# Performance work log

Measured on AMD Instinct MI355X. Metric: run time of the kernel, lower is better.

## Reference

```python
import jax, jax.numpy as jnp
import numpy as np

GROUPSIZE = 4      # g: multivariate group size (d = groupsize - 2)
NB_GROUPS = 48     # f: number of expert groups / filters
CHANNELS = 128     # c: signal channels fed to the L operator
SCALE = 0.999
SLOPE = 1.0        # model_params['scaling']
LAMB_INIT = 0.1
EPS_OMEGA_INIT = -2.0


def proj_l1(x):
    """Euclidean projection onto the unit l1 ball along axis 1. x: [B,G,F,H,W]."""
    ax = jnp.abs(x)
    s = -jnp.sort(-ax, axis=1)                      # descending |x|
    cssv = jnp.cumsum(s, axis=1) - 1.0
    G = x.shape[1]
    k = jnp.arange(1, G + 1, dtype=x.dtype).reshape(1, G, 1, 1, 1)
    cond = s * k > cssv
    rho = jnp.sum(cond, axis=1, keepdims=True)       # number of active coords
    theta = jnp.take_along_axis(cssv, rho - 1, axis=1) / rho.astype(x.dtype)
    theta = jnp.maximum(theta, 0.0)
    proj = jnp.sign(x) * jnp.maximum(ax - theta, 0.0)
    inside = jnp.sum(ax, axis=1, keepdims=True) <= 1.0
    return jnp.where(inside, x, proj)


def _forward(x_noisy, sigma, Q_param, taus_param, lamb, eps_omega,
             mu_w1, mu_b1, mu_w2, mu_b2, mu_w3, mu_b3, Wf, n_iter):
    lamb_e = jnp.exp(lamb)
    eps_e = jnp.exp(eps_omega)

    # --- Q normalization + spectral norms (cached once per forward) ---
    Q = Q_param / jnp.maximum(jnp.sum(jnp.abs(Q_param), axis=2, keepdims=True), 1.0)
    Q_norms = jnp.linalg.svd(Q, compute_uv=False)[:, 0].reshape(-1, 1, 1)  # [F,1,1]
    Q_eff = Q / Q_norms ** 2
    taus = jnp.exp(jax.nn.relu(taus_param))          # [1,1,F,1,1]

    # --- per-batch noise-adaptive scaling via small MLP ---
    h = jax.nn.relu((sigma * 20.0 - 2.0) @ mu_w1 + mu_b1)
    h = jax.nn.relu(h @ mu_w2 + mu_b2)
    h = h @ mu_w3 + mu_b3                            # [B,F]
    scaling = jax.nn.relu(h * 0.05 + sigma) * SLOPE + 1e-9
    scaling = scaling.reshape(-1, 1, scaling.shape[-1], 1, 1)  # [B,1,F,1,1]

    def moreau(x):
        g = proj_l1(x)
        cost = jnp.max(jnp.abs(x - g), axis=1) + 0.5 * jnp.sum(g * g, axis=1)
        cost = cost[:, None]                         # [B,1,F,H,W]
        g = g + eps_e * x
        cost = cost + eps_e * 0.5 * jnp.sqrt(jnp.sum(x * x, axis=1, keepdims=True))
        return g, cost

    def activation(x):
        gc, cc = moreau(x)
        # orient: scale * einsum('flg,bgfhw->blfhw', Q/Q_norms^2, x), then /taus
        y = SCALE * jnp.einsum('flg,bgfhw->blfhw', Q_eff, x) / taus
        gcc, ccc = moreau(y)
        # unorient: scale * einsum with Q^T  (Q^T[f,l,g] = Q[f,g,l])
        gcc = SCALE * jnp.einsum('fgl,bgfhw->blfhw', Q, gcc)
        ccc = Q_norms ** 2 * (taus * ccc)
        return lamb_e * (gc - gcc), lamb_e * (cc - ccc)

    def reconstruct(x):
        Lx = jnp.einsum('gfc,bchw->bgfhw', Wf, x) / scaling
        g, cost = activation(Lx)
        g = jnp.einsum('gfc,bgfhw->bchw', Wf, g * scaling)   # adjoint L^T
        cost = jnp.sum(cost * scaling ** 2, axis=(1, 2, 3, 4))
        g = (x - x_noisy + g) / (1.0 + lamb_e * (1.0 + eps_e))
        cost = cost + 0.5 * jnp.sum((x - x_noisy) ** 2, axis=(1, 2, 3))
        return g, cost

    def step(x, _):
        g, _c = reconstruct(x)
        return x - g, None

    x_final, _ = jax.lax.scan(jax.checkpoint(step), x_noisy, jnp.arange(n_iter))
    return x_final


def setup_inputs() -> dict:
    key = jax.random.key(0)
    ks = jax.random.split(key, 8)
    B, C, H, W = 2, CHANNELS, 128, 128
    F_, G = NB_GROUPS, GROUPSIZE
    x_noisy = jax.random.normal(ks[0], (B, C, H, W), jnp.float32)
    sigma = jax.random.uniform(ks[1], (B, 1), jnp.float32)
    Q_param = jax.random.uniform(ks[2], (F_, G, G), jnp.float32) - 0.5
    taus_param = (LAMB_INIT / 2.0) * jnp.ones((1, 1, F_, 1, 1), jnp.float32)
    lamb = jnp.float32(LAMB_INIT)
    eps_omega = jnp.float32(EPS_OMEGA_INIT)
    mu_w1 = jax.random.normal(ks[3], (1, F_), jnp.float32)
    mu_b1 = jnp.zeros((F_,), jnp.float32)
    mu_w2 = jax.random.normal(ks[4], (F_, F_), jnp.float32) / np.float32(np.sqrt(F_))
    mu_b2 = jnp.zeros((F_,), jnp.float32)
    mu_w3 = jax.random.normal(ks[5], (F_, F_), jnp.float32) / np.float32(np.sqrt(F_))
    mu_b3 = jnp.zeros((F_,), jnp.float32)
    Wf = jax.random.normal(ks[6], (G, F_, C), jnp.float32) / np.float32(np.sqrt(C))
    return dict(x_noisy=x_noisy, sigma=sigma, Q_param=Q_param, taus_param=taus_param,
                lamb=lamb, eps_omega=eps_omega, mu_w1=mu_w1, mu_b1=mu_b1,
                mu_w2=mu_w2, mu_b2=mu_b2, mu_w3=mu_w3, mu_b3=mu_b3, Wf=Wf, n_iter=10)


def reference(x_noisy, sigma, Q_param, taus_param, lamb, eps_omega,
              mu_w1, mu_b1, mu_w2, mu_b2, mu_w3, mu_b3, Wf, n_iter):
    return _forward(x_noisy, sigma, Q_param, taus_param, lamb, eps_omega,
                    mu_w1, mu_b1, mu_w2, mu_b2, mu_w3, mu_b3, Wf, n_iter)
```

## Files before the change

### kernel.cpp

```cpp
#include <hip/hip_runtime.h>
#include <math.h>

#define F_ 48
#define C_ 128
#define HW 16384
#define SCALE_C 0.999f
#define TPB 256
#define MTPB 512

typedef __attribute__((ext_vector_type(8))) short short8;
typedef __attribute__((ext_vector_type(4))) float floatx4;
typedef __attribute__((ext_vector_type(8))) _Float16 half8;
typedef __attribute__((ext_vector_type(4))) _Float16 half4;

#define P1_U 0
#define P2_U 98304
#define QEQN_F 98304
#define MISC_F (QEQN_F + 1536)
#define SINV_F (MISC_F + 2)
#define SLAM_F (SINV_F + 96)

#define QS 36

__device__ __forceinline__ unsigned short f2bf(float f) {
    unsigned u = __float_as_uint(f);
    unsigned r = u + 0x7fffu + ((u >> 16) & 1u);
    return (unsigned short)(r >> 16);
}
__device__ __forceinline__ float bf2f(unsigned short h) {
    return __uint_as_float(((unsigned)h) << 16);
}

__global__ void setup_math(const float* __restrict__ sigma,
                           const float* __restrict__ Qp,
                           const float* __restrict__ taus_p,
                           const float* __restrict__ lamb,
                           const float* __restrict__ eps_om,
                           const float* __restrict__ mw1, const float* __restrict__ mb1,
                           const float* __restrict__ mw2, const float* __restrict__ mb2,
                           const float* __restrict__ mw3, const float* __restrict__ mb3,
                           float* __restrict__ wsf)
{
    const int tid = threadIdx.x;
    if (tid < F_) {
        const int f = tid;
        float Qm[4][4];
        for (int g = 0; g < 4; ++g) {
            float s = 0.f;
            for (int l = 0; l < 4; ++l) s += fabsf(Qp[f * 16 + g * 4 + l]);
            float d = fmaxf(s, 1.0f);
            for (int l = 0; l < 4; ++l) Qm[g][l] = Qp[f * 16 + g * 4 + l] / d;
        }
        double A[4][4];
        for (int i = 0; i < 4; ++i)
            for (int j = 0; j < 4; ++j) {
                double s = 0.0;
                for (int g = 0; g < 4; ++g) s += (double)Qm[g][i] * (double)Qm[g][j];
                A[i][j] = s;
            }
        double M[4][4];
        for (int i = 0; i < 4; ++i) for (int j = 0; j < 4; ++j) M[i][j] = A[i][j];
        for (int it = 0; it < 30; ++it) {
            double T[4][4]; double mx = 0.0;
            for (int i = 0; i < 4; ++i)
                for (int j = 0; j < 4; ++j) {
                    double s = 0.0;
                    for (int k = 0; k < 4; ++k) s += M[i][k] * M[k][j];
                    T[i][j] = s;
                    double a = fabs(s); if (a > mx) mx = a;
                }
            if (mx < 1e-300) break;
            double inv = 1.0 / mx;
            for (int i = 0; i < 4; ++i) for (int j = 0; j < 4; ++j) M[i][j] = T[i][j] * inv;
        }
        int jb = 0; double bn = -1.0;
        for (int j = 0; j < 4; ++j) {
            double nn = 0.0;
            for (int i = 0; i < 4; ++i) nn += M[i][j] * M[i][j];
            if (nn > bn) { bn = nn; jb = j; }
        }
        double v[4]; for (int i = 0; i < 4; ++i) v[i] = M[i][jb];
        double Av[4];
        for (int i = 0; i < 4; ++i) {
            double s = 0.0;
            for (int j = 0; j < 4; ++j) s += A[i][j] * v[j];
            Av[i] = s;
        }
        double vv = 0.0, vav = 0.0;
        for (int i = 0; i < 4; ++i) { vv += v[i] * v[i]; vav += v[i] * Av[i]; }
        float lamf = (float)((vv > 0.0) ? (vav / vv) : 0.0);
        float tau = expf(fmaxf(taus_p[f], 0.0f));
        float qsv = SCALE_C / tau;
        for (int l = 0; l < 4; ++l)
            for (int g = 0; g < 4; ++g)
                wsf[QEQN_F + f * 32 + l * 4 + g] = qsv * Qm[l][g] / lamf;
        for (int g = 0; g < 4; ++g)
            for (int l = 0; l < 4; ++l)
                wsf[QEQN_F + f * 32 + 16 + g * 4 + l] = SCALE_C * Qm[g][l];
    }
    if (tid >= 48 && tid < 50) {
        const int b = tid - 48;
        float lamb_e = expf(lamb[0]);
        float sg = sigma[b];
        float t = sg * 20.0f - 2.0f;
        float h1[F_], h2[F_];
        for (int j = 0; j < F_; ++j) h1[j] = fmaxf(t * mw1[j] + mb1[j], 0.0f);
        for (int j = 0; j < F_; ++j) {
            float s = mb2[j];
            for (int k = 0; k < F_; ++k) s += h1[k] * mw2[k * F_ + j];
            h2[j] = fmaxf(s, 0.0f);
        }
        for (int j = 0; j < F_; ++j) {
            float s = mb3[j];
            for (int k = 0; k < F_; ++k) s += h2[k] * mw3[k * F_ + j];
            float sc = fmaxf(s * 0.05f + sg, 0.0f) + 1e-9f;
            wsf[SINV_F + b * F_ + j] = 1.0f / sc;
            wsf[SLAM_F + b * F_ + j] = lamb_e * sc;
        }
    }
    if (tid == 50) {
        float lamb_e = expf(lamb[0]);
        float eps_e = expf(eps_om[0]);
        wsf[MISC_F + 0] = eps_e;
        wsf[MISC_F + 1] = 1.0f / (1.0f + lamb_e * (1.0f + eps_e));
    }
}

__global__ void setup_pack(const float* __restrict__ Wf, float* __restrict__ wsf)
{
    unsigned short* wsu = (unsigned short*)wsf;
    const int gtid = blockIdx.x * TPB + threadIdx.x;
    for (int i = gtid; i < 49152; i += gridDim.x * TPB) {
        if (i < 24576) {
            int j = i & 7, lane = (i >> 3) & 63;
            int t = i >> 9;
            int ks = t & 3, mt = t >> 2;
            int m = lane & 15, q = lane >> 4;
            int r = mt * 16 + m;
            int c = ks * 32 + q * 8 + j;
            int f = r >> 2, g = r & 3;
            float w = Wf[(g * F_ + f) * C_ + c];
            _Float16 hv = (_Float16)w;
            wsu[P1_U + ((mt * 4 + ks) * 64 + lane) * 8 + j] = *(unsigned short*)&hv;
        } else {
            int ii = i - 24576;
            int j = ii & 7, lane = (ii >> 3) & 63;
            int t = ii >> 9;
            int ks = t % 6, cmt = t / 6;
            int m = lane & 15, q = lane >> 4;
            int cch = cmt * 16 + m;
            int r = ks * 32 + q * 8 + j;
            int g = r & 3;
            int f = r >> 2;
            float w = Wf[(g * F_ + f) * C_ + cch];
            _Float16 hv = (_Float16)w;
            wsu[P2_U + ((cmt * 6 + ks) * 64 + lane) * 8 + j] = *(unsigned short*)&hv;
        }
    }
}

__device__ __forceinline__ void proj4(const float v[4], float o[4]) {
    float a0 = fabsf(v[0]), a1 = fabsf(v[1]), a2 = fabsf(v[2]), a3 = fabsf(v[3]);
    float sum = a0 + a1 + a2 + a3;
    float t0 = fmaxf(a0, a1), u0 = fminf(a0, a1);
    float t1 = fmaxf(a2, a3), u1 = fminf(a2, a3);
    float s0 = fmaxf(t0, t1), m0 = fminf(t0, t1);
    float m1 = fmaxf(u0, u1), s3 = fminf(u0, u1);
    float s1 = fmaxf(m1, m0), s2 = fminf(m1, m0);
    float c2 = s0 + s1, c3 = c2 + s2, c4 = c3 + s3;
    float th = s0 - 1.0f, rh = 1.0f;
    if (s1 * 2.0f > c2 - 1.0f) { th = c2 - 1.0f; rh = 2.0f; }
    if (s2 * 3.0f > c3 - 1.0f) { th = c3 - 1.0f; rh = 3.0f; }
    if (s3 * 4.0f > c4 - 1.0f) { th = c4 - 1.0f; rh = 4.0f; }
    float theta = fmaxf(th / rh, 0.0f);
    bool inside = (sum <= 1.0f);
#pragma unroll
    for (int g = 0; g < 4; ++g) {
        float ag = fabsf(v[g]);
        float pg = copysignf(fmaxf(ag - theta, 0.0f), v[g]);
        o[g] = inside ? v[g] : pg;
    }
}

__global__ __launch_bounds__(MTPB, 4) void mfoe_main(
    const float* __restrict__ xnoisy,
    const float* __restrict__ wsf,
    float* __restrict__ out,
    const int* __restrict__ n_iter_p)
{
    __shared__ __align__(16) _Float16 sXF[4096];
    __shared__ __align__(16) _Float16 sACT[6144];
    __shared__ __align__(16) float sQ[F_ * QS];

    const int tid = threadIdx.x;
    const int lane = tid & 63;
    const int wv = __builtin_amdgcn_readfirstlane(tid >> 6);
    const int n = lane & 15;
    const int q = lane >> 4;
    const int blk = blockIdx.x;
    const int b = blk >> 9;
    const int pix0 = (blk & 511) << 5;

    const float* __restrict__ xin = xnoisy + b * (C_ * HW) + pix0;
    float* __restrict__ oimg = out + b * (C_ * HW) + pix0;
    const unsigned short* __restrict__ wsu = (const unsigned short*)wsf;
    const int niter = *n_iter_p;

    if (niter == 0) {
        for (int i = tid; i < C_ * 32; i += MTPB) {
            int p = i & 31, c = i >> 5;
            oimg[c * HW + p] = xin[c * HW + p];
        }
        return;
    }

    for (int i = tid; i < C_ * 32; i += MTPB) {
        int p = i & 31, c = i >> 5;
        int idx = ((p >> 4) * 4 + (c >> 5)) * 512 + (((c >> 3) & 3) * 16 + (p & 15)) * 8 + (c & 7);
        sXF[idx] = (_Float16)xin[c * HW + p];
    }
    for (int i = tid; i < F_ * 32; i += MTPB)
        sQ[(i >> 5) * QS + (i & 31)] = wsf[QEQN_F + i];
    for (int i = tid; i < F_; i += MTPB) {
        sQ[i * QS + 32] = wsf[SINV_F + b * F_ + i];
        sQ[i * QS + 33] = wsf[SLAM_F + b * F_ + i];
    }

    float xnr[8];
#pragma unroll
    for (int j = 0; j < 2; ++j) {
        int jw = wv * 2 + j, cmt = jw >> 1, nt = jw & 1;
        int p = nt * 16 + n;
#pragma unroll
        for (int reg = 0; reg < 4; ++reg)
            xnr[j * 4 + reg] = xin[(cmt * 16 + q * 4 + reg) * HW + p];
    }
    const float eps_e = wsf[MISC_F + 0];
    const float invden = wsf[MISC_F + 1];

    for (int it = 0; it < niter; ++it) {
        __syncthreads();
#pragma unroll 1
        for (int j = 0; j < 3; ++j) {
            int jw = wv * 3 + j, mt = jw >> 1, nt = jw & 1;
            floatx4 acc = (floatx4){0.f, 0.f, 0.f, 0.f};
            const half8* aFp = (const half8*)(wsu + P1_U + (mt * 4) * 512 + lane * 8);
            const half8* bFp = (const half8*)&sXF[nt * 2048 + lane * 8];
#pragma unroll
            for (int ks = 0; ks < 4; ++ks) {
                half8 aF = aFp[ks * 64];
                half8 bF = bFp[ks * 64];
                acc = __builtin_amdgcn_mfma_f32_16x16x32_f16(aF, bF, acc, 0, 0, 0);
            }
            int f = mt * 4 + q;
            float qv[32];
#pragma unroll
            for (int k = 0; k < 8; ++k)
                *(floatx4*)&qv[4 * k] = *(const floatx4*)&sQ[f * QS + 4 * k];
            float invs = sQ[f * QS + 32];
            float slam = sQ[f * QS + 33];
            float v[4] = {acc[0] * invs, acc[1] * invs, acc[2] * invs, acc[3] * invs};
            float pv[4]; proj4(v, pv);
            float y[4];
#pragma unroll
            for (int l = 0; l < 4; ++l)
                y[l] = fmaf(qv[l * 4 + 0], v[0], fmaf(qv[l * 4 + 1], v[1],
                       fmaf(qv[l * 4 + 2], v[2], qv[l * 4 + 3] * v[3])));
            float py[4]; proj4(y, py);
            float m2[4];
#pragma unroll
            for (int g = 0; g < 4; ++g) m2[g] = fmaf(eps_e, y[g], py[g]);
            half4 av;
            {
                float gcc0 = fmaf(qv[16 + 0], m2[0], fmaf(qv[16 + 4], m2[1],
                             fmaf(qv[16 + 8], m2[2], qv[16 + 12] * m2[3])));
                av[0] = (_Float16)((fmaf(eps_e, v[0], pv[0]) - gcc0) * slam);
                float gcc1 = fmaf(qv[17 + 0], m2[0], fmaf(qv[17 + 4], m2[1],
                             fmaf(qv[17 + 8], m2[2], qv[17 + 12] * m2[3])));
                av[1] = (_Float16)((fmaf(eps_e, v[1], pv[1]) - gcc1) * slam);
                float gcc2 = fmaf(qv[18 + 0], m2[0], fmaf(qv[18 + 4], m2[1],
                             fmaf(qv[18 + 8], m2[2], qv[18 + 12] * m2[3])));
                av[2] = (_Float16)((fmaf(eps_e, v[2], pv[2]) - gcc2) * slam);
                float gcc3 = fmaf(qv[19 + 0], m2[0], fmaf(qv[19 + 4], m2[1],
                             fmaf(qv[19 + 8], m2[2], qv[19 + 12] * m2[3])));
                av[3] = (_Float16)((fmaf(eps_e, v[3], pv[3]) - gcc3) * slam);
            }
            int aw = ((nt * 6 + (mt >> 1)) * 64 + ((mt & 1) * 2 + (q >> 1)) * 16 + n) * 8 + (q & 1) * 4;
            *(half4*)&sACT[aw] = av;
        }
        __syncthreads();
        floatx4 acc2[2];
#pragma unroll
        for (int j = 0; j < 2; ++j) acc2[j] = (floatx4){0.f, 0.f, 0.f, 0.f};
#pragma unroll
        for (int j = 0; j < 2; ++j) {
            int jw = wv * 2 + j, cmt = jw >> 1, nt = jw & 1;
            const half8* a2F = (const half8*)(wsu + P2_U + ((cmt * 6) * 64) * 8 + lane * 8);
            const half8* bAp = (const half8*)&sACT[nt * 3072 + lane * 8];
            floatx4 a = acc2[j];
#pragma unroll
            for (int ks = 0; ks < 6; ++ks) {
                half8 aF = a2F[ks * 64];
                half8 bA = bAp[ks * 64];
                a = __builtin_amdgcn_mfma_f32_16x16x32_f16(aF, bA, a, 0, 0, 0);
            }
            acc2[j] = a;
        }
        const bool last = (it == niter - 1);
#pragma unroll
        for (int j = 0; j < 2; ++j) {
            int jw = wv * 2 + j, cmt = jw >> 1, nt = jw & 1;
            int p = nt * 16 + n;
            int cb = cmt * 16 + q * 4;
            int xu = ((nt * 4 + (cmt >> 1)) * 64 + ((cmt & 1) * 2 + (q >> 1)) * 16 + n) * 8 + (q & 1) * 4;
            half4 xo4 = *(const half4*)&sXF[xu];
            float xo0 = (float)xo4[0];
            float xo1 = (float)xo4[1];
            float xo2 = (float)xo4[2];
            float xo3 = (float)xo4[3];
            float nx0 = xo0 - ((xo0 - xnr[j * 4 + 0]) + acc2[j][0]) * invden;
            float nx1 = xo1 - ((xo1 - xnr[j * 4 + 1]) + acc2[j][1]) * invden;
            float nx2 = xo2 - ((xo2 - xnr[j * 4 + 2]) + acc2[j][2]) * invden;
            float nx3 = xo3 - ((xo3 - xnr[j * 4 + 3]) + acc2[j][3]) * invden;
            if (last) {
                oimg[(cb + 0) * HW + p] = nx0;
                oimg[(cb + 1) * HW + p] = nx1;
                oimg[(cb + 2) * HW + p] = nx2;
                oimg[(cb + 3) * HW + p] = nx3;
            }
            half4 nx4;
            nx4[0] = (_Float16)nx0;
            nx4[1] = (_Float16)nx1;
            nx4[2] = (_Float16)nx2;
            nx4[3] = (_Float16)nx3;
            *(half4*)&sXF[xu] = nx4;
        }
    }
}

extern "C" void kernel_launch(void* const* d_in, const int* in_sizes, int n_in,
                              void* d_out, int out_size, void* d_ws, size_t ws_size,
                              hipStream_t stream) {
    const float* x_noisy = (const float*)d_in[0];
    const float* sigma   = (const float*)d_in[1];
    const float* Qp      = (const float*)d_in[2];
    const float* taus_p  = (const float*)d_in[3];
    const float* lamb    = (const float*)d_in[4];
    const float* eps_om  = (const float*)d_in[5];
    const float* mw1     = (const float*)d_in[6];
    const float* mb1     = (const float*)d_in[7];
    const float* mw2     = (const float*)d_in[8];
    const float* mb2     = (const float*)d_in[9];
    const float* mw3     = (const float*)d_in[10];
    const float* mb3     = (const float*)d_in[11];
    const float* Wf      = (const float*)d_in[12];
    const int*   n_iter  = (const int*)d_in[13];
    float* out = (float*)d_out;
    float* ws  = (float*)d_ws;

    hipLaunchKernelGGL(setup_math, dim3(1), dim3(64), 0, stream,
                       sigma, Qp, taus_p, lamb, eps_om,
                       mw1, mb1, mw2, mb2, mw3, mb3, ws);
    hipLaunchKernelGGL(setup_pack, dim3(192), dim3(TPB), 0, stream, Wf, ws);
    hipLaunchKernelGGL(mfoe_main, dim3(1024), dim3(MTPB), 0, stream,
                       x_noisy, ws, out, n_iter);
}
```

Baseline: 267.9 us.

## Fold Q orientation into packed weights, doubling MFMA work to drop per-pixel 4x4 matmuls

Precomputes Q·Wf and -Qᵀ·Wf in setup_pack and stores them as extra fp16 MFMA weight tiles. The main kernel then gets y directly from a second MFMA accumulator, and the back-projection of the oriented branch is folded into a wider second GEMM with K=384. This removes the per-lane 4x4 Q matmuls, the 32-float Q register loads from shared memory, and a division in proj4. In exchange it doubles the first-GEMM MFMAs and the second-GEMM K, doubles the shared activation buffer, and rounds Q-folded weights to fp16, which may change accuracy.

After: 287.0 us. 1.07x slower.

```diff
diff --git a/kernel.cpp b/kernel.cpp
--- a/kernel.cpp
+++ b/kernel.cpp
@@ -8,28 +8,16 @@
 #define TPB 256
 #define MTPB 512
 
-typedef __attribute__((ext_vector_type(8))) short short8;
 typedef __attribute__((ext_vector_type(4))) float floatx4;
 typedef __attribute__((ext_vector_type(8))) _Float16 half8;
 typedef __attribute__((ext_vector_type(4))) _Float16 half4;
 
 #define P1_U 0
-#define P2_U 98304
-#define QEQN_F 98304
+#define P2_U 49152
+#define QEQN_F 49152
 #define MISC_F (QEQN_F + 1536)
 #define SINV_F (MISC_F + 2)
 #define SLAM_F (SINV_F + 96)
-
-#define QS 36
-
-__device__ __forceinline__ unsigned short f2bf(float f) {
-    unsigned u = __float_as_uint(f);
-    unsigned r = u + 0x7fffu + ((u >> 16) & 1u);
-    return (unsigned short)(r >> 16);
-}
-__device__ __forceinline__ float bf2f(unsigned short h) {
-    return __uint_as_float(((unsigned)h) << 16);
-}
 
 __global__ void setup_math(const float* __restrict__ sigma,
                            const float* __restrict__ Qp,
@@ -130,31 +118,48 @@
 {
     unsigned short* wsu = (unsigned short*)wsf;
     const int gtid = blockIdx.x * TPB + threadIdx.x;
-    for (int i = gtid; i < 49152; i += gridDim.x * TPB) {
-        if (i < 24576) {
+    for (int i = gtid; i < 98304; i += gridDim.x * TPB) {
+        if (i < 49152) {
             int j = i & 7, lane = (i >> 3) & 63;
             int t = i >> 9;
-            int ks = t & 3, mt = t >> 2;
-            int m = lane & 15, q = lane >> 4;
-            int r = mt * 16 + m;
-            int c = ks * 32 + q * 8 + j;
-            int f = r >> 2, g = r & 3;
-            float w = Wf[(g * F_ + f) * C_ + c];
+            int ks = t & 3, mtile = t >> 2;
+            int rt = lane & 15, qq = lane >> 4;
+            int c = ks * 32 + qq * 8 + j;
+            int ft = mtile >> 1;
+            int f = ft * 4 + (rt >> 2);
+            int gl = rt & 3;
+            float w;
+            if ((mtile & 1) == 0) {
+                w = Wf[(gl * F_ + f) * C_ + c];
+            } else {
+                w = 0.f;
+                for (int g = 0; g < 4; ++g)
+                    w += wsf[QEQN_F + f * 32 + gl * 4 + g] * Wf[(g * F_ + f) * C_ + c];
+            }
             _Float16 hv = (_Float16)w;
-            wsu[P1_U + ((mt * 4 + ks) * 64 + lane) * 8 + j] = *(unsigned short*)&hv;
+            wsu[P1_U + ((mtile * 4 + ks) * 64 + lane) * 8 + j] = *(unsigned short*)&hv;
         } else {
-            int ii = i - 24576;
+            int ii = i - 49152;
             int j = ii & 7, lane = (ii >> 3) & 63;
             int t = ii >> 9;
-            int ks = t % 6, cmt = t / 6;
-            int m = lane & 15, q = lane >> 4;
+            int ks = t % 12, cmt = t / 12;
+            int m = lane & 15, qq = lane >> 4;
             int cch = cmt * 16 + m;
-            int r = ks * 32 + q * 8 + j;
-            int g = r & 3;
-            int f = r >> 2;
-            float w = Wf[(g * F_ + f) * C_ + cch];
+            int r = ks * 32 + qq * 8 + j;
+            float w;
+            if (ks < 6) {
+                int f = r >> 2, g = r & 3;
+                w = Wf[(g * F_ + f) * C_ + cch];
+            } else {
+                int rp = r - 192;
+                int f = rp >> 2, l = rp & 3;
+                w = 0.f;
+                for (int g = 0; g < 4; ++g)
+                    w += wsf[QEQN_F + f * 32 + 16 + l * 4 + g] * Wf[(g * F_ + f) * C_ + cch];
+                w = -w;
+            }
             _Float16 hv = (_Float16)w;
-            wsu[P2_U + ((cmt * 6 + ks) * 64 + lane) * 8 + j] = *(unsigned short*)&hv;
+            wsu[P2_U + ((cmt * 12 + ks) * 64 + lane) * 8 + j] = *(unsigned short*)&hv;
         }
     }
 }
@@ -168,11 +173,11 @@
     float m1 = fmaxf(u0, u1), s3 = fminf(u0, u1);
     float s1 = fmaxf(m1, m0), s2 = fminf(m1, m0);
     float c2 = s0 + s1, c3 = c2 + s2, c4 = c3 + s3;
-    float th = s0 - 1.0f, rh = 1.0f;
-    if (s1 * 2.0f > c2 - 1.0f) { th = c2 - 1.0f; rh = 2.0f; }
-    if (s2 * 3.0f > c3 - 1.0f) { th = c3 - 1.0f; rh = 3.0f; }
-    if (s3 * 4.0f > c4 - 1.0f) { th = c4 - 1.0f; rh = 4.0f; }
-    float theta = fmaxf(th / rh, 0.0f);
+    float th = s0 - 1.0f, rs = 1.0f;
+    if (s1 * 2.0f > c2 - 1.0f) { th = c2 - 1.0f; rs = 0.5f; }
+    if (s2 * 3.0f > c3 - 1.0f) { th = c3 - 1.0f; rs = (1.0f / 3.0f); }
+    if (s3 * 4.0f > c4 - 1.0f) { th = c4 - 1.0f; rs = 0.25f; }
+    float theta = fmaxf(th * rs, 0.0f);
     bool inside = (sum <= 1.0f);
 #pragma unroll
     for (int g = 0; g < 4; ++g) {
@@ -189,8 +194,8 @@
     const int* __restrict__ n_iter_p)
 {
     __shared__ __align__(16) _Float16 sXF[4096];
-    __shared__ __align__(16) _Float16 sACT[6144];
-    __shared__ __align__(16) float sQ[F_ * QS];
+    __shared__ __align__(16) _Float16 sACT[12288];
+    __shared__ __align__(16) float sISL[96];
 
     const int tid = threadIdx.x;
     const int lane = tid & 63;
@@ -219,11 +224,9 @@
         int idx = ((p >> 4) * 4 + (c >> 5)) * 512 + (((c >> 3) & 3) * 16 + (p & 15)) * 8 + (c & 7);
         sXF[idx] = (_Float16)xin[c * HW + p];
     }
-    for (int i = tid; i < F_ * 32; i += MTPB)
-        sQ[(i >> 5) * QS + (i & 31)] = wsf[QEQN_F + i];
-    for (int i = tid; i < F_; i += MTPB) {
-        sQ[i * QS + 32] = wsf[SINV_F + b * F_ + i];
-        sQ[i * QS + 33] = wsf[SLAM_F + b * F_ + i];
+    for (int i = tid; i < 96; i += MTPB) {
+        if (i < 48) sISL[i] = wsf[SINV_F + b * F_ + i];
+        else        sISL[i] = wsf[SLAM_F + b * F_ + (i - 48)];
     }
 
     float xnr[8];
@@ -242,51 +245,33 @@
         __syncthreads();
 #pragma unroll 1
         for (int j = 0; j < 3; ++j) {
-            int jw = wv * 3 + j, mt = jw >> 1, nt = jw & 1;
-            floatx4 acc = (floatx4){0.f, 0.f, 0.f, 0.f};
-            const half8* aFp = (const half8*)(wsu + P1_U + (mt * 4) * 512 + lane * 8);
+            int jw = wv * 3 + j, ft = jw >> 1, nt = jw & 1;
+            floatx4 accv = (floatx4){0.f, 0.f, 0.f, 0.f};
+            floatx4 accy = (floatx4){0.f, 0.f, 0.f, 0.f};
+            const half8* aE = (const half8*)(wsu + P1_U + (ft * 8) * 512 + lane * 8);
             const half8* bFp = (const half8*)&sXF[nt * 2048 + lane * 8];
 #pragma unroll
             for (int ks = 0; ks < 4; ++ks) {
-                half8 aF = aFp[ks * 64];
                 half8 bF = bFp[ks * 64];
-                acc = __builtin_amdgcn_mfma_f32_16x16x32_f16(aF, bF, acc, 0, 0, 0);
-            }
-            int f = mt * 4 + q;
-            float qv[32];
-#pragma unroll
-            for (int k = 0; k < 8; ++k)
-                *(floatx4*)&qv[4 * k] = *(const floatx4*)&sQ[f * QS + 4 * k];
-            float invs = sQ[f * QS + 32];
-            float slam = sQ[f * QS + 33];
-            float v[4] = {acc[0] * invs, acc[1] * invs, acc[2] * invs, acc[3] * invs};
+                accv = __builtin_amdgcn_mfma_f32_16x16x32_f16(aE[ks * 64], bF, accv, 0, 0, 0);
+                accy = __builtin_amdgcn_mfma_f32_16x16x32_f16(aE[ks * 64 + 256], bF, accy, 0, 0, 0);
+            }
+            int f = ft * 4 + q;
+            float invs = sISL[f];
+            float slam = sISL[48 + f];
+            float v[4] = {accv[0] * invs, accv[1] * invs, accv[2] * invs, accv[3] * invs};
+            float y[4] = {accy[0] * invs, accy[1] * invs, accy[2] * invs, accy[3] * invs};
             float pv[4]; proj4(v, pv);
-            float y[4];
-#pragma unroll
-            for (int l = 0; l < 4; ++l)
-                y[l] = fmaf(qv[l * 4 + 0], v[0], fmaf(qv[l * 4 + 1], v[1],
-                       fmaf(qv[l * 4 + 2], v[2], qv[l * 4 + 3] * v[3])));
             float py[4]; proj4(y, py);
-            float m2[4];
-#pragma unroll
-            for (int g = 0; g < 4; ++g) m2[g] = fmaf(eps_e, y[g], py[g]);
-            half4 av;
-            {
-                float gcc0 = fmaf(qv[16 + 0], m2[0], fmaf(qv[16 + 4], m2[1],
-                             fmaf(qv[16 + 8], m2[2], qv[16 + 12] * m2[3])));
-                av[0] = (_Float16)((fmaf(eps_e, v[0], pv[0]) - gcc0) * slam);
-                float gcc1 = fmaf(qv[17 + 0], m2[0], fmaf(qv[17 + 4], m2[1],
-                             fmaf(qv[17 + 8], m2[2], qv[17 + 12] * m2[3])));
-                av[1] = (_Float16)((fmaf(eps_e, v[1], pv[1]) - gcc1) * slam);
-                float gcc2 = fmaf(qv[18 + 0], m2[0], fmaf(qv[18 + 4], m2[1],
-                             fmaf(qv[18 + 8], m2[2], qv[18 + 12] * m2[3])));
-                av[2] = (_Float16)((fmaf(eps_e, v[2], pv[2]) - gcc2) * slam);
-                float gcc3 = fmaf(qv[19 + 0], m2[0], fmaf(qv[19 + 4], m2[1],
-                             fmaf(qv[19 + 8], m2[2], qv[19 + 12] * m2[3])));
-                av[3] = (_Float16)((fmaf(eps_e, v[3], pv[3]) - gcc3) * slam);
-            }
-            int aw = ((nt * 6 + (mt >> 1)) * 64 + ((mt & 1) * 2 + (q >> 1)) * 16 + n) * 8 + (q & 1) * 4;
-            *(half4*)&sACT[aw] = av;
+            half4 au, am;
+#pragma unroll
+            for (int g = 0; g < 4; ++g) {
+                au[g] = (_Float16)(fmaf(eps_e, v[g], pv[g]) * slam);
+                am[g] = (_Float16)(fmaf(eps_e, y[g], py[g]) * slam);
+            }
+            int aw = ((nt * 12 + (ft >> 1)) * 64 + ((ft & 1) * 2 + (q >> 1)) * 16 + n) * 8 + (q & 1) * 4;
+            *(half4*)&sACT[aw] = au;
+            *(half4*)&sACT[aw + 3072] = am;
         }
         __syncthreads();
         floatx4 acc2[2];
@@ -295,11 +280,11 @@
 #pragma unroll
         for (int j = 0; j < 2; ++j) {
             int jw = wv * 2 + j, cmt = jw >> 1, nt = jw & 1;
-            const half8* a2F = (const half8*)(wsu + P2_U + ((cmt * 6) * 64) * 8 + lane * 8);
-            const half8* bAp = (const half8*)&sACT[nt * 3072 + lane * 8];
+            const half8* a2F = (const half8*)(wsu + P2_U + (cmt * 12) * 512 + lane * 8);
+            const half8* bAp = (const half8*)&sACT[nt * 6144 + lane * 8];
             floatx4 a = acc2[j];
 #pragma unroll
-            for (int ks = 0; ks < 6; ++ks) {
+            for (int ks = 0; ks < 12; ++ks) {
                 half8 aF = a2F[ks * 64];
                 half8 bA = bAp[ks * 64];
                 a = __builtin_amdgcn_mfma_f32_16x16x32_f16(aF, bA, a, 0, 0, 0);
```
